# Kernel tuning notes

Hardware: AMD Instinct MI355X
Metric: run time of the kernel (lower is better)

Reference implementation:

```python
import jax, jax.numpy as jnp
import numpy as np
from jax import lax

B, IN_N, MID_N, OUT_N, K, L, WH = 16, 256, 256, 256, 3, 4096, 1024
EPS = 1e-5


def att_conv(x, W, b=None):
    # x: [B, Cin, L], W: [B, Cout, Cin, K] -> per-sample conv1d, padding='same'
    pl, pr = (K - 1) // 2, K // 2
    xp = jnp.pad(x, ((0, 0), (0, 0), (pl, pr)))
    out = 0.
    for t in range(K):  # small fixed K, unrolled shifted-slice einsum
        out = out + jnp.einsum('bcl,boc->bol', lax.dynamic_slice_in_dim(xp, t, L, 2), W[..., t])
    if b is not None:
        out = out + b[:, :, None]
    return out


def batch_norm(x, w, b):
    # training-mode BN over (N, L) per channel, biased variance
    mean = x.mean((0, 2), keepdims=True)
    var = ((x - mean) ** 2).mean((0, 2), keepdims=True)
    return (x - mean) * (w[None, :, None] / jnp.sqrt(var + EPS)) + b[None, :, None]


def se_module(x, w1, b1, w2, b2):
    s = x.mean(2, keepdims=True)  # [B, C, 1]
    s = jax.nn.relu(jnp.einsum('bcl,oc->bol', s, w1) + b1[None, :, None])
    s = jax.nn.sigmoid(jnp.einsum('bcl,oc->bol', s, w2) + b2[None, :, None])
    return x * s


def setup_inputs() -> dict:
    key = jax.random.key(0)
    ks = jax.random.split(key, 16)
    f = lambda k, sh, sc=0.02: jax.random.normal(k, sh, jnp.float32) * sc
    return {
        'x': f(ks[0], (B, IN_N, L), 1.0),
        'att1': f(ks[1], (B, MID_N, WH), 1.0),
        'att2': f(ks[2], (B, MID_N, WH), 1.0),
        'att3': f(ks[3], (B, OUT_N, WH), 1.0),
        'w1_w': f(ks[4], (IN_N * K, WH)), 'w1_b': jnp.zeros((IN_N * K,), jnp.float32),
        'w2_w': f(ks[5], (MID_N * K, WH)), 'w2_b': jnp.zeros((MID_N * K,), jnp.float32),
        'w3_w': f(ks[6], (MID_N * K, WH)), 'w3_b': jnp.zeros((MID_N * K,), jnp.float32),
        'b1_w': f(ks[7], (1, WH)), 'b1_b': jnp.zeros((1,), jnp.float32),
        'bn2_w': jnp.full((MID_N,), 0.1, jnp.float32), 'bn2_b': jnp.zeros((MID_N,), jnp.float32),
        'bn3_w': jnp.full((OUT_N,), 0.1, jnp.float32), 'bn3_b': jnp.zeros((OUT_N,), jnp.float32),
        'se1_w': f(ks[8], (OUT_N, OUT_N)), 'se1_b': jnp.zeros((OUT_N,), jnp.float32),
        'se2_w': f(ks[9], (OUT_N, OUT_N)), 'se2_b': jnp.zeros((OUT_N,), jnp.float32),
    }


def reference(x, att1, att2, att3, w1_w, w1_b, w2_w, w2_b, w3_w, w3_b,
              b1_w, b1_b, bn2_w, bn2_b, bn3_w, bn3_b, se1_w, se1_b, se2_w, se2_b):
    shortcut = x  # in_n == out_n, no downsample -> Identity
    # hypernetwork weight generation (Linear on last dim)
    W1 = (att1 @ w1_w.T + w1_b).reshape(B, MID_N, IN_N, K)
    W2 = (att2 @ w2_w.T + w2_b).reshape(B, MID_N, MID_N, K)
    W3 = (att3 @ w3_w.T + w3_b).reshape(B, OUT_N, MID_N, K)
    b1 = (att1 @ b1_w.T + b1_b)[..., 0]  # [B, mid_n]
    h = jax.nn.relu(att_conv(x, W1, b1))
    h = jax.nn.relu(batch_norm(att_conv(h, W2), bn2_w, bn2_b))
    h = jax.nn.relu(batch_norm(att_conv(h, W3), bn3_w, bn3_b))
    out = jax.nn.relu(se_module(h, se1_w, se1_b, se2_w, se2_b) + shortcut)
    return out
```

## Files before the change

### kernel.cpp

```cpp
#include <hip/hip_runtime.h>
#include <hip/hip_bf16.h>

using bf16 = __hip_bfloat16;
typedef __attribute__((ext_vector_type(4))) float f32x4;
typedef __attribute__((ext_vector_type(8))) short short8;
typedef __attribute__((ext_vector_type(2))) unsigned int uint2v;
typedef __attribute__((ext_vector_type(4))) unsigned int uint4v;

#define DEVI static __device__ __forceinline__

DEVI unsigned short f2b(float f){
  unsigned int u = __float_as_uint(f);
  unsigned int r = (u + 0x7fffu + ((u >> 16) & 1u)) >> 16;
  return (unsigned short)r;
}
DEVI float b2f(unsigned short u){
  return __uint_as_float(((unsigned int)u) << 16);
}

DEVI void gload16(const void* g, void* l){
  __builtin_amdgcn_global_load_lds(
      (const __attribute__((address_space(1))) unsigned int*)g,
      (__attribute__((address_space(3))) unsigned int*)l, 16, 0, 0);
}

__global__ __launch_bounds__(256) void k_transpose_x(const float* __restrict__ x,
                                                     bf16* __restrict__ xt)
{
  __shared__ float tile[64][65];
  const int b = blockIdx.z, l0 = blockIdx.x*64, c0 = blockIdx.y*64;
  const int tid = threadIdx.x;
  {
    const int r = tid >> 2, q = tid & 3;
    const float* src = x + ((size_t)(b*256 + c0 + r))*4096 + l0 + q*16;
    #pragma unroll
    for (int j = 0; j < 4; ++j){
      const f32x4 v = *reinterpret_cast<const f32x4*>(src + j*4);
      #pragma unroll
      for (int e = 0; e < 4; ++e) tile[r][q*16 + j*4 + e] = v[e];
    }
  }
  __syncthreads();
  {
    const int jr = tid >> 2, cq = tid & 3;
    unsigned int w[8];
    #pragma unroll
    for (int e = 0; e < 8; ++e){
      const float lo = tile[cq*16 + 2*e][jr];
      const float hi = tile[cq*16 + 2*e + 1][jr];
      w[e] = (unsigned int)f2b(lo) | ((unsigned int)f2b(hi) << 16);
    }
    unsigned short* dst = (unsigned short*)xt + ((size_t)b*4098 + l0 + jr + 1)*256 + c0 + cq*16;
    uint4v a0 = {w[0],w[1],w[2],w[3]}, a1 = {w[4],w[5],w[6],w[7]};
    *reinterpret_cast<uint4v*>(dst)     = a0;
    *reinterpret_cast<uint4v*>(dst + 8) = a1;
  }
}

__global__ void k_zero_pads(bf16* __restrict__ xt, bf16* __restrict__ h1t)
{
  const int b = blockIdx.x, tid = threadIdx.x;
  const size_t top = (size_t)b*4098*256 + tid;
  const size_t bot = (size_t)b*4098*256 + (size_t)4097*256 + tid;
  unsigned short* px = (unsigned short*)xt;
  unsigned short* ph = (unsigned short*)h1t;
  px[top] = 0; px[bot] = 0; ph[top] = 0; ph[bot] = 0;
}

__global__ __launch_bounds__(256) void k_cvt3(const float* __restrict__ s0, const float* __restrict__ s1,
                                              const float* __restrict__ s2, bf16* __restrict__ dst, int n1)
{
  const size_t total = (size_t)3 * (size_t)n1 / 4;
  for (size_t i = (size_t)blockIdx.x*256 + threadIdx.x; i < total; i += (size_t)gridDim.x*256){
    const size_t e = i*4;
    const int which = (int)(e / (size_t)n1);
    const size_t off = e - (size_t)which*(size_t)n1;
    const float* s = which==0 ? s0 : which==1 ? s1 : s2;
    const f32x4 v = *reinterpret_cast<const f32x4*>(s + off);
    uint2v p;
    p[0] = (unsigned)f2b(v[0]) | ((unsigned)f2b(v[1])<<16);
    p[1] = (unsigned)f2b(v[2]) | ((unsigned)f2b(v[3])<<16);
    *reinterpret_cast<uint2v*>((unsigned short*)dst + e) = p;
  }
}

__global__ __launch_bounds__(256, 3) void k_gen(const float* __restrict__ att1f, const float* __restrict__ att2f,
                                                const float* __restrict__ att3f, const bf16* __restrict__ wbp,
                                                const float* __restrict__ bias0, const float* __restrict__ bias1,
                                                const float* __restrict__ bias2, bf16* __restrict__ Wt)
{
  __shared__ bf16 sAll[24576];
  const int flat = blockIdx.x + blockIdx.z*64;
  const int xcd = flat & 7, s = flat >> 3;
  const int t = s % 3, u = s / 3;
  const int ch = u & 1;
  const int tau = (u >> 1)*8 + xcd;
  const int i = tau >> 5, boc = tau & 31;
  const int bo0 = boc*128, c0 = ch*128;
  const bf16*  __restrict__ A  = wbp + (size_t)i*768*1024 + (size_t)(c0*3 + t)*1024;
  const float* __restrict__ Bf = ((i==0) ? att1f : (i==1) ? att2f : att3f) + (size_t)bo0*1024;
  const float* __restrict__ bias = (i==0) ? bias0 : (i==1) ? bias1 : bias2;
  const int tid = threadIdx.x, lane = tid & 63, wid = tid >> 6;
  const int wr = wid >> 1, wc = wid & 1;
  const int frow = lane & 15, g = lane >> 4;
  f32x4 acc[4][4] = {};

#define GEN_STAGE(kt, bufi) { \
    _Pragma("unroll") \
    for (int j = 0; j < 2; ++j){ \
      const int q = tid + j*256, r = q >> 2, s3 = q & 3; \
      const int cc = (s3 ^ ((r >> 1) & 3)) * 8; \
      gload16(A + (size_t)r*3072 + (kt)*32 + cc, (char*)sAll + (bufi)*8192 + q*16); \
    } \
    _Pragma("unroll") \
    for (int j = 0; j < 4; ++j){ \
      const int q = tid + j*256, r = q >> 3, s7 = q & 7; \
      const int ss = s7 ^ (r & 7); \
      gload16(Bf + (size_t)r*1024 + (kt)*32 + ss*4, (char*)sAll + 16384 + (bufi)*16384 + q*16); \
    } \
  }

  GEN_STAGE(0, 0);
  #pragma unroll 1
  for (int kt = 0; kt < 32; ++kt){
    const int p = kt & 1;
    if (kt + 1 < 32){
      GEN_STAGE(kt+1, p^1);
      asm volatile("s_waitcnt vmcnt(6)" ::: "memory");
    } else {
      asm volatile("s_waitcnt vmcnt(0)" ::: "memory");
    }
    __builtin_amdgcn_s_barrier();
    const char* pA = (const char*)sAll + p*8192;
    const char* pB = (const char*)sAll + 16384 + p*16384;
    short8 bfr[4];
    #pragma unroll
    for (int n = 0; n < 4; ++n){
      const int row = wc*64 + n*16 + frow;
      const f32x4 f0 = *reinterpret_cast<const f32x4*>(pB + row*128 + (((2*g)  ^ (row & 7))*16));
      const f32x4 f1 = *reinterpret_cast<const f32x4*>(pB + row*128 + (((2*g+1)^ (row & 7))*16));
      unsigned int w0, w1, w2, w3;
      asm("v_cvt_pk_bf16_f32 %0, %1, %2" : "=v"(w0) : "v"(f0[0]), "v"(f0[1]));
      asm("v_cvt_pk_bf16_f32 %0, %1, %2" : "=v"(w1) : "v"(f0[2]), "v"(f0[3]));
      asm("v_cvt_pk_bf16_f32 %0, %1, %2" : "=v"(w2) : "v"(f1[0]), "v"(f1[1]));
      asm("v_cvt_pk_bf16_f32 %0, %1, %2" : "=v"(w3) : "v"(f1[2]), "v"(f1[3]));
      union { uint4v u; short8 sv; } cvtu;
      cvtu.u[0] = w0; cvtu.u[1] = w1; cvtu.u[2] = w2; cvtu.u[3] = w3;
      bfr[n] = cvtu.sv;
    }
    __builtin_amdgcn_s_setprio(1);
    #pragma unroll
    for (int m = 0; m < 4; ++m){
      const int row = wr*64 + m*16 + frow;
      const int sl = g ^ ((row >> 1) & 3);
      const short8 af = *reinterpret_cast<const short8*>(pA + row*64 + sl*16);
      #pragma unroll
      for (int n = 0; n < 4; ++n)
        acc[m][n] = __builtin_amdgcn_mfma_f32_16x16x32_bf16(af, bfr[n], acc[m][n], 0, 0, 0);
    }
    __builtin_amdgcn_s_setprio(0);
    __builtin_amdgcn_s_barrier();
  }
#undef GEN_STAGE

  #pragma unroll
  for (int m = 0; m < 4; ++m){
    const int lcol = wr*64 + m*16 + g*4;
    float bi[4];
    #pragma unroll
    for (int j = 0; j < 4; ++j) bi[j] = bias[(c0 + lcol + j)*3 + t];
    #pragma unroll
    for (int n = 0; n < 4; ++n){
      const int row = wc*64 + n*16 + frow;
      uint2v pk;
      pk[0] = (unsigned)f2b(acc[m][n][0] + bi[0]) | ((unsigned)f2b(acc[m][n][1] + bi[1]) << 16);
      pk[1] = (unsigned)f2b(acc[m][n][2] + bi[2]) | ((unsigned)f2b(acc[m][n][3] + bi[3]) << 16);
      const int chunk = (lcol >> 3) ^ (row & 15);
      *reinterpret_cast<uint2v*>((char*)sAll + row*256 + chunk*16 + (g&1)*8) = pk;
    }
  }
  __syncthreads();
  {
    const int bb = boc >> 1, o0 = (boc & 1)*128;
    char* gp = (char*)Wt + 2*(((((size_t)(i*16 + bb)*3 + t)*256 + o0)*256) + c0);
    #pragma unroll
    for (int it = 0; it < 8; ++it){
      const int row = it*16 + (tid >> 4);
      const int c = tid & 15;
      const int cs2 = c ^ (row & 15);
      const uint4v v = *reinterpret_cast<const uint4v*>((const char*)sAll + row*256 + cs2*16);
      *reinterpret_cast<uint4v*>(gp + (size_t)row*512 + c*16) = v;
    }
  }
}

__global__ __launch_bounds__(256) void k_b1(const float* __restrict__ att1, const float* __restrict__ b1w,
                                            const float* __restrict__ b1b, float* __restrict__ out)
{
  const int m = blockIdx.x*4 + (threadIdx.x >> 6);
  const int lane = threadIdx.x & 63;
  const float* a = att1 + (size_t)m*1024;
  float s = 0.f;
  for (int k = lane*4; k < 1024; k += 256){
    const f32x4 v = *reinterpret_cast<const f32x4*>(a + k);
    const f32x4 w = *reinterpret_cast<const f32x4*>(b1w + k);
    s += v[0]*w[0] + v[1]*w[1] + v[2]*w[2] + v[3]*w[3];
  }
  #pragma unroll
  for (int d = 32; d > 0; d >>= 1) s += __shfl_down(s, d);
  if (lane == 0) out[m] = s + b1b[0];
}

__global__ __launch_bounds__(512, 4) void k_conv(const bf16* __restrict__ Xt, const bf16* __restrict__ W,
                                                 const float* __restrict__ bias, bf16* __restrict__ out,
                                                 int outBatchStride, int outRowOff, int applyRelu,
                                                 float* __restrict__ statSum, float* __restrict__ statSq)
{
  __shared__ bf16 sAll[32768];
  const int flat = blockIdx.x + (blockIdx.z << 5);
  const int xcd = flat & 7, slot = flat >> 3;
  const int b = 2*xcd + (slot >> 5);
  const int l0 = (slot & 31) * 128;
  const int tid = threadIdx.x, lane = tid & 63, wid = tid >> 6;
  const int wr = wid >> 1, wc = wid & 1;
  const int frow = lane & 15, g = lane >> 4;
  f32x4 acc[4][4] = {};

#define CONV_STAGE(kt, bufi) { \
    const int ct3 = (kt)/3, tt = (kt) - ct3*3, c0 = ct3*32; \
    const bf16* Ab = W  + (((size_t)b*3 + tt)*256)*256 + c0; \
    const bf16* Bb = Xt + ((size_t)b*4098 + l0 + tt)*256 + c0; \
    _Pragma("unroll") \
    for (int j = 0; j < 2; ++j){ \
      const int q = tid + j*512, r = q >> 2, s3 = q & 3; \
      const int cc = (s3 ^ ((r >> 1) & 3)) * 8; \
      gload16(Ab + (size_t)r*256 + cc, &sAll[(bufi)*8192 + q*8]); \
    } \
    { const int q = tid, r = q >> 2, s3 = q & 3; \
      const int cc = (s3 ^ ((r >> 1) & 3)) * 8; \
      gload16(Bb + (size_t)r*256 + cc, &sAll[16384 + (bufi)*4096 + q*8]); } \
  }

  CONV_STAGE(0, 0);
  #pragma unroll 1
  for (int kt = 0; kt < 24; ++kt){
    const int buf = kt & 1;
    if (kt + 1 < 24){
      CONV_STAGE(kt+1, buf^1);
      asm volatile("s_waitcnt vmcnt(3)" ::: "memory");
    } else {
      asm volatile("s_waitcnt vmcnt(0)" ::: "memory");
    }
    __builtin_amdgcn_s_barrier();
    const bf16* pA = sAll + buf*8192;
    const bf16* pB = sAll + 16384 + buf*4096;
    short8 bfr[4], afr[4];
    #pragma unroll
    for (int n = 0; n < 4; ++n){
      const int row = wc*64 + n*16 + frow;
      const int sl = g ^ ((row >> 1) & 3);
      bfr[n] = *reinterpret_cast<const short8*>(pB + row*32 + sl*8);
    }
    #pragma unroll
    for (int m = 0; m < 4; ++m){
      const int row = wr*64 + m*16 + frow;
      const int sl = g ^ ((row >> 1) & 3);
      afr[m] = *reinterpret_cast<const short8*>(pA + row*32 + sl*8);
    }
    __builtin_amdgcn_s_setprio(1);
    #pragma unroll
    for (int m = 0; m < 4; ++m)
      #pragma unroll
      for (int n = 0; n < 4; ++n)
        acc[m][n] = __builtin_amdgcn_mfma_f32_16x16x32_bf16(afr[m], bfr[n], acc[m][n], 0, 0, 0);
    __builtin_amdgcn_s_setprio(0);
    __builtin_amdgcn_s_barrier();
  }
#undef CONV_STAGE

  float cs[4][4] = {{0.f}}, cq[4][4] = {{0.f}};
  #pragma unroll
  for (int m = 0; m < 4; ++m){
    const int col = wr*64 + m*16 + g*4;
    float bi[4] = {0.f, 0.f, 0.f, 0.f};
    if (bias){
      const f32x4 bv = *reinterpret_cast<const f32x4*>(bias + b*256 + col);
      bi[0]=bv[0]; bi[1]=bv[1]; bi[2]=bv[2]; bi[3]=bv[3];
    }
    #pragma unroll
    for (int n = 0; n < 4; ++n){
      const int row = wc*64 + n*16 + frow;
      float v[4];
      #pragma unroll
      for (int j = 0; j < 4; ++j){
        v[j] = acc[m][n][j] + bi[j];
        if (applyRelu) v[j] = fmaxf(v[j], 0.f);
        cs[m][j] += v[j];
        cq[m][j] += v[j]*v[j];
      }
      uint2v pk;
      pk[0] = (unsigned)f2b(v[0]) | ((unsigned)f2b(v[1]) << 16);
      pk[1] = (unsigned)f2b(v[2]) | ((unsigned)f2b(v[3]) << 16);
      const int chunk = (col >> 3) ^ (row & 31);
      *reinterpret_cast<uint2v*>((char*)sAll + row*512 + chunk*16 + (g&1)*8) = pk;
    }
  }
  __syncthreads();
  {
    char* gp = (char*)out + 2*((size_t)b*outBatchStride + (size_t)(l0 + outRowOff)*256);
    #pragma unroll
    for (int it = 0; it < 8; ++it){
      const int row = it*16 + (tid >> 5);
      const int c = tid & 31;
      const int cs2 = c ^ (row & 31);
      const uint4v v = *reinterpret_cast<const uint4v*>((const char*)sAll + row*512 + cs2*16);
      *reinterpret_cast<uint4v*>(gp + (size_t)row*512 + c*16) = v;
    }
  }
  if (statSum){
    #pragma unroll
    for (int m = 0; m < 4; ++m)
      #pragma unroll
      for (int j = 0; j < 4; ++j){
        #pragma unroll
        for (int d = 1; d < 16; d <<= 1){
          cs[m][j] += __shfl_xor(cs[m][j], d);
          cq[m][j] += __shfl_xor(cq[m][j], d);
        }
      }
    __syncthreads();
    float* ls = (float*)sAll;
    float* lq = ls + 512;
    if (frow == 0){
      #pragma unroll
      for (int m = 0; m < 4; ++m)
        #pragma unroll
        for (int j = 0; j < 4; ++j){
          ls[wid*64 + m*16 + g*4 + j] = cs[m][j];
          lq[wid*64 + m*16 + g*4 + j] = cq[m][j];
        }
    }
    __syncthreads();
    if (tid < 256){
      const int o = tid, wrI = o >> 6, idx = o & 63;
      const float s  = ls[(wrI*2 + 0)*64 + idx] + ls[(wrI*2 + 1)*64 + idx];
      const float qq = lq[(wrI*2 + 0)*64 + idx] + lq[(wrI*2 + 1)*64 + idx];
      atomicAdd(statSum + o, s);
      atomicAdd(statSq  + o, qq);
    }
  }
}

__global__ void k_bnfin(const float* __restrict__ sum, const float* __restrict__ sq,
                        const float* __restrict__ g, const float* __restrict__ bb,
                        float* __restrict__ scale, float* __restrict__ shift)
{
  const int o = threadIdx.x;
  const float inv = 1.f/65536.f;
  const float m = sum[o]*inv;
  const float v = fmaxf(sq[o]*inv - m*m, 0.f);
  const float sc = g[o] / sqrtf(v + 1e-5f);
  scale[o] = sc;
  shift[o] = bb[o] - m*sc;
}

__global__ __launch_bounds__(256) void k_norm2(const bf16* __restrict__ y, const float* __restrict__ scale,
                                               const float* __restrict__ shift, bf16* __restrict__ h)
{
  const int gr = blockIdx.x*8 + (threadIdx.x >> 5);
  const int oc = threadIdx.x & 31;
  const int b = gr / 4098, lp = gr - b*4098;
  unsigned short* dst = (unsigned short*)h + (size_t)gr*256 + oc*8;
  if (lp == 0 || lp == 4097){
    uint4v z = {0u,0u,0u,0u};
    *reinterpret_cast<uint4v*>(dst) = z;
    return;
  }
  const unsigned short* src = (const unsigned short*)y + ((size_t)b*4096 + (lp-1))*256 + oc*8;
  const uint4v in = *reinterpret_cast<const uint4v*>(src);
  const f32x4 sA0 = *reinterpret_cast<const f32x4*>(scale + oc*8);
  const f32x4 sA1 = *reinterpret_cast<const f32x4*>(scale + oc*8 + 4);
  const f32x4 hA0 = *reinterpret_cast<const f32x4*>(shift + oc*8);
  const f32x4 hA1 = *reinterpret_cast<const f32x4*>(shift + oc*8 + 4);
  uint4v ov;
  #pragma unroll
  for (int e = 0; e < 4; ++e){
    const unsigned int w = in[e];
    const float sc0 = (e<2) ? sA0[2*e] : sA1[2*e-4];
    const float sc1 = (e<2) ? sA0[2*e+1] : sA1[2*e-3];
    const float sh0 = (e<2) ? hA0[2*e] : hA1[2*e-4];
    const float sh1 = (e<2) ? hA0[2*e+1] : hA1[2*e-3];
    const float v0 = fmaxf(b2f((unsigned short)(w & 0xffffu))*sc0 + sh0, 0.f);
    const float v1 = fmaxf(b2f((unsigned short)(w >> 16))*sc1 + sh1, 0.f);
    ov[e] = (unsigned)f2b(v0) | ((unsigned)f2b(v1) << 16);
  }
  *reinterpret_cast<uint4v*>(dst) = ov;
}

__global__ __launch_bounds__(256) void k_norm3(bf16* __restrict__ y, const float* __restrict__ scale,
                                               const float* __restrict__ shift, float* __restrict__ s_sum)
{
  __shared__ float red[8][256];
  const int tid = threadIdx.x;
  const int rr = tid >> 5, oc = tid & 31;
  const size_t row = (size_t)blockIdx.x*8 + rr;
  const int b = (int)(row >> 12);
  unsigned short* p = (unsigned short*)y + row*256 + oc*8;
  const uint4v in = *reinterpret_cast<const uint4v*>(p);
  const f32x4 sA0 = *reinterpret_cast<const f32x4*>(scale + oc*8);
  const f32x4 sA1 = *reinterpret_cast<const f32x4*>(scale + oc*8 + 4);
  const f32x4 hA0 = *reinterpret_cast<const f32x4*>(shift + oc*8);
  const f32x4 hA1 = *reinterpret_cast<const f32x4*>(shift + oc*8 + 4);
  uint4v ov;
  float loc[8];
  #pragma unroll
  for (int e = 0; e < 4; ++e){
    const unsigned int w = in[e];
    const float sc0 = (e<2) ? sA0[2*e] : sA1[2*e-4];
    const float sc1 = (e<2) ? sA0[2*e+1] : sA1[2*e-3];
    const float sh0 = (e<2) ? hA0[2*e] : hA1[2*e-4];
    const float sh1 = (e<2) ? hA0[2*e+1] : hA1[2*e-3];
    const float v0 = fmaxf(b2f((unsigned short)(w & 0xffffu))*sc0 + sh0, 0.f);
    const float v1 = fmaxf(b2f((unsigned short)(w >> 16))*sc1 + sh1, 0.f);
    loc[2*e] = v0; loc[2*e+1] = v1;
    ov[e] = (unsigned)f2b(v0) | ((unsigned)f2b(v1) << 16);
  }
  *reinterpret_cast<uint4v*>(p) = ov;
  #pragma unroll
  for (int j = 0; j < 8; ++j) red[rr][oc*8 + j] = loc[j];
  __syncthreads();
  const int o = tid;
  float tot = 0.f;
  #pragma unroll
  for (int r2 = 0; r2 < 8; ++r2) tot += red[r2][o];
  atomicAdd(&s_sum[(size_t)b*256 + o], tot);
}

__global__ __launch_bounds__(256) void k_se(const float* __restrict__ s_sum, const float* __restrict__ w1,
                                            const float* __restrict__ b1, const float* __restrict__ w2,
                                            const float* __restrict__ b2, float* __restrict__ s2)
{
  __shared__ float sv[256];
  __shared__ float t1[256];
  const int b = blockIdx.x, o = threadIdx.x;
  sv[o] = s_sum[(size_t)b*256 + o] * (1.f/4096.f);
  __syncthreads();
  float a = b1[o];
  for (int c = 0; c < 256; ++c) a += w1[(size_t)o*256 + c] * sv[c];
  t1[o] = fmaxf(a, 0.f);
  __syncthreads();
  float a2 = b2[o];
  for (int c = 0; c < 256; ++c) a2 += w2[(size_t)o*256 + c] * t1[c];
  s2[(size_t)b*256 + o] = 1.f / (1.f + expf(-a2));
}

__global__ __launch_bounds__(256) void k_final(const bf16* __restrict__ h3, const float* __restrict__ s2,
                                               const float* __restrict__ x, float* __restrict__ out)
{
  __shared__ float tile[64][65];
  const int b = blockIdx.z, o0 = blockIdx.y*64, l0 = blockIdx.x*64;
  const int tid = threadIdx.x;
  {
    const int r = tid >> 2, q = tid & 3;
    const unsigned short* src = (const unsigned short*)h3 + ((size_t)b*4096 + l0 + r)*256 + o0 + q*16;
    const uint4v a0 = *reinterpret_cast<const uint4v*>(src);
    const uint4v a1 = *reinterpret_cast<const uint4v*>(src + 8);
    #pragma unroll
    for (int e = 0; e < 4; ++e){
      tile[r][q*16 + 2*e]         = b2f((unsigned short)(a0[e] & 0xffffu));
      tile[r][q*16 + 2*e + 1]     = b2f((unsigned short)(a0[e] >> 16));
      tile[r][q*16 + 8 + 2*e]     = b2f((unsigned short)(a1[e] & 0xffffu));
      tile[r][q*16 + 8 + 2*e + 1] = b2f((unsigned short)(a1[e] >> 16));
    }
  }
  __syncthreads();
  {
    const int orow = tid >> 2, q = tid & 3;
    const int o = o0 + orow;
    const float sc = s2[(size_t)b*256 + o];
    const float* xs = x + ((size_t)b*256 + o)*4096 + l0 + q*16;
    float* dst = out + ((size_t)b*256 + o)*4096 + l0 + q*16;
    #pragma unroll
    for (int k = 0; k < 16; k += 4){
      const f32x4 xv = *reinterpret_cast<const f32x4*>(xs + k);
      f32x4 r;
      #pragma unroll
      for (int e = 0; e < 4; ++e)
        r[e] = fmaxf(tile[q*16 + k + e][orow]*sc + xv[e], 0.f);
      *reinterpret_cast<f32x4*>(dst + k) = r;
    }
  }
}

extern "C" void kernel_launch(void* const* d_in, const int* in_sizes, int n_in,
                              void* d_out, int out_size, void* d_ws, size_t ws_size,
                              hipStream_t stream)
{
  const float* x     = (const float*)d_in[0];
  const float* att1  = (const float*)d_in[1];
  const float* att2  = (const float*)d_in[2];
  const float* att3  = (const float*)d_in[3];
  const float* w1_w  = (const float*)d_in[4];
  const float* w1_b  = (const float*)d_in[5];
  const float* w2_w  = (const float*)d_in[6];
  const float* w2_b  = (const float*)d_in[7];
  const float* w3_w  = (const float*)d_in[8];
  const float* w3_b  = (const float*)d_in[9];
  const float* b1_w  = (const float*)d_in[10];
  const float* b1_b  = (const float*)d_in[11];
  const float* bn2_w = (const float*)d_in[12];
  const float* bn2_b = (const float*)d_in[13];
  const float* bn3_w = (const float*)d_in[14];
  const float* bn3_b = (const float*)d_in[15];
  const float* se1_w = (const float*)d_in[16];
  const float* se1_b = (const float*)d_in[17];
  const float* se2_w = (const float*)d_in[18];
  const float* se2_b = (const float*)d_in[19];

  char* ws = (char*)d_ws;
  bf16*  xT   = (bf16*)(ws + 0);
  bf16*  h1T  = (bf16*)(ws + 33570816);
  bf16*  y2T  = (bf16*)(ws + 67141632);
  bf16*  h2T  = (bf16*)(ws + 100696064);
  bf16*  Wt   = (bf16*)(ws + 134266880);
  bf16*  wb   = (bf16*)(ws + 178307072);
  float* b1v  = (float*)(ws + 183025664);
  float* st   = (float*)(ws + 183042048);
  float* bn2sum = st;
  float* bn2sq  = st + 256;
  float* bn3sum = st + 512;
  float* bn3sq  = st + 768;
  float* s_sum  = st + 1024;
  float* scale2 = st + 5120;
  float* shift2 = st + 5376;
  float* scale3 = st + 5632;
  float* shift3 = st + 5888;
  float* s2v    = st + 6144;
  bf16*  y3T  = (bf16*)(ws + 0);

  hipMemsetAsync(st, 0, 5120*sizeof(float), stream);

  k_transpose_x<<<dim3(64,4,16),256,0,stream>>>(x, xT);
  k_zero_pads<<<16,256,0,stream>>>(xT, h1T);
  k_cvt3<<<512,256,0,stream>>>(w1_w, w2_w, w3_w, wb, 768*1024);
  k_gen<<<dim3(64,1,9),256,0,stream>>>(att1, att2, att3, wb, w1_b, w2_b, w3_b, Wt);
  k_b1<<<1024,256,0,stream>>>(att1, b1_w, b1_b, b1v);

  k_conv<<<dim3(32,1,16),512,0,stream>>>(xT,  Wt,                           b1v,     h1T, 4098*256, 1, 1, nullptr, nullptr);
  k_conv<<<dim3(32,1,16),512,0,stream>>>(h1T, Wt + (size_t)1*16*3*256*256,  nullptr, y2T, 4096*256, 0, 0, bn2sum, bn2sq);
  k_bnfin<<<1,256,0,stream>>>(bn2sum, bn2sq, bn2_w, bn2_b, scale2, shift2);
  k_norm2<<<8196,256,0,stream>>>(y2T, scale2, shift2, h2T);
  k_conv<<<dim3(32,1,16),512,0,stream>>>(h2T, Wt + (size_t)2*16*3*256*256,  nullptr, y3T, 4096*256, 0, 0, bn3sum, bn3sq);
  k_bnfin<<<1,256,0,stream>>>(bn3sum, bn3sq, bn3_w, bn3_b, scale3, shift3);
  k_norm3<<<8192,256,0,stream>>>(y3T, scale3, shift3, s_sum);
  k_se<<<16,256,0,stream>>>(s_sum, se1_w, se1_b, se2_w, se2_b, s2v);
  k_final<<<dim3(64,4,16),256,0,stream>>>((const bf16*)y3T, s2v, x, (float*)d_out);
}
```

Baseline: 309.2 us.

## Enlarge conv tile to 256x256 with 64-wide K steps and interleaved staging

Result: no change. 307.6 us (-0.5%).

```diff
diff --git a/kernel.cpp b/kernel.cpp
--- a/kernel.cpp
+++ b/kernel.cpp
@@ -211,77 +211,106 @@
   if (lane == 0) out[m] = s + b1b[0];
 }
 
-__global__ __launch_bounds__(512, 4) void k_conv(const bf16* __restrict__ Xt, const bf16* __restrict__ W,
+__global__ __launch_bounds__(512, 2) void k_conv(const bf16* __restrict__ Xt, const bf16* __restrict__ W,
                                                  const float* __restrict__ bias, bf16* __restrict__ out,
                                                  int outBatchStride, int outRowOff, int applyRelu,
                                                  float* __restrict__ statSum, float* __restrict__ statSq)
 {
-  __shared__ bf16 sAll[32768];
-  const int flat = blockIdx.x + (blockIdx.z << 5);
-  const int xcd = flat & 7, slot = flat >> 3;
-  const int b = 2*xcd + (slot >> 5);
-  const int l0 = (slot & 31) * 128;
+  __shared__ bf16 sAll[65536];
+  const int flat = blockIdx.x + (blockIdx.z << 4);
+  const int xcd = flat & 7, sl_ = flat >> 3;
+  const int b = 2*xcd + (sl_ >> 4);
+  const int l0 = (sl_ & 15) * 256;
   const int tid = threadIdx.x, lane = tid & 63, wid = tid >> 6;
-  const int wr = wid >> 1, wc = wid & 1;
+  const int wr = wid >> 2, wc = wid & 3;
   const int frow = lane & 15, g = lane >> 4;
-  f32x4 acc[4][4] = {};
-
-#define CONV_STAGE(kt, bufi) { \
-    const int ct3 = (kt)/3, tt = (kt) - ct3*3, c0 = ct3*32; \
-    const bf16* Ab = W  + (((size_t)b*3 + tt)*256)*256 + c0; \
-    const bf16* Bb = Xt + ((size_t)b*4098 + l0 + tt)*256 + c0; \
+  f32x4 acc[8][4] = {};
+
+  const int r0 = tid >> 3,        cc0 = ((tid & 7) ^ (r0 & 7));
+  const int r1 = (tid+512) >> 3,  cc1 = (((tid+512) & 7) ^ (r1 & 7));
+
+#define BARR asm volatile("s_barrier" ::: "memory")
+
+#define STG_A(j, h) { const int t_=(j)%3, c0_=((j)/3)*64; \
+    const bf16* gp_ = W + (((size_t)b*3 + t_)*256 + (h)*128)*256 + c0_; \
+    char* lb_ = (char*)sAll + (((j)&1)*32768) + (h)*16384; \
+    gload16(gp_ + (size_t)r0*256 + cc0*8, lb_ + tid*16); \
+    gload16(gp_ + (size_t)r1*256 + cc1*8, lb_ + (tid+512)*16); }
+
+#define STG_B(j, h) { const int t_=(j)%3, c0_=((j)/3)*64; \
+    const bf16* gp_ = Xt + ((size_t)b*4098 + l0 + t_ + (h)*128)*256 + c0_; \
+    char* lb_ = (char*)sAll + 65536 + (((j)&1)*32768) + (h)*16384; \
+    gload16(gp_ + (size_t)r0*256 + cc0*8, lb_ + tid*16); \
+    gload16(gp_ + (size_t)r1*256 + cc1*8, lb_ + (tid+512)*16); }
+
+#define RD_A(j, mh) { const char* pa_ = (const char*)sAll + (((j)&1)*32768) + wr*16384; \
     _Pragma("unroll") \
-    for (int j = 0; j < 2; ++j){ \
-      const int q = tid + j*512, r = q >> 2, s3 = q & 3; \
-      const int cc = (s3 ^ ((r >> 1) & 3)) * 8; \
-      gload16(Ab + (size_t)r*256 + cc, &sAll[(bufi)*8192 + q*8]); \
-    } \
-    { const int q = tid, r = q >> 2, s3 = q & 3; \
-      const int cc = (s3 ^ ((r >> 1) & 3)) * 8; \
-      gload16(Bb + (size_t)r*256 + cc, &sAll[16384 + (bufi)*4096 + q*8]); } \
-  }
-
-  CONV_STAGE(0, 0);
+    for (int mf = 0; mf < 4; ++mf){ const int rowl = ((mh)*4 + mf)*16 + frow; \
+      _Pragma("unroll") \
+      for (int ks = 0; ks < 2; ++ks) \
+        afr[mf][ks] = *reinterpret_cast<const short8*>(pa_ + rowl*128 + (((ks*4+g) ^ (rowl & 7))*16)); } }
+
+#define RD_B(j) { const char* pb_ = (const char*)sAll + 65536 + (((j)&1)*32768) + (wc>>1)*16384; \
+    _Pragma("unroll") \
+    for (int nf = 0; nf < 4; ++nf){ const int rowl = (wc&1)*64 + nf*16 + frow; \
+      _Pragma("unroll") \
+      for (int ks = 0; ks < 2; ++ks) \
+        bfr[nf][ks] = *reinterpret_cast<const short8*>(pb_ + rowl*128 + (((ks*4+g) ^ (rowl & 7))*16)); } }
+
+#define MFMA16(mh, ks) { __builtin_amdgcn_s_setprio(1); \
+    _Pragma("unroll") \
+    for (int mf = 0; mf < 4; ++mf) \
+      _Pragma("unroll") \
+      for (int nf = 0; nf < 4; ++nf) \
+        acc[(mh)*4+mf][nf] = __builtin_amdgcn_mfma_f32_16x16x32_bf16(afr[mf][ks], bfr[nf][ks], acc[(mh)*4+mf][nf], 0, 0, 0); \
+    __builtin_amdgcn_s_setprio(0); }
+
+  STG_A(0,0); STG_A(0,1); STG_B(0,0); STG_B(0,1);
+  STG_A(1,0); STG_A(1,1); STG_B(1,0); STG_B(1,1);
+  asm volatile("s_waitcnt vmcnt(0)" ::: "memory");
+  BARR;
+
+  short8 afr[4][2], bfr[4][2];
   #pragma unroll 1
-  for (int kt = 0; kt < 24; ++kt){
-    const int buf = kt & 1;
-    if (kt + 1 < 24){
-      CONV_STAGE(kt+1, buf^1);
-      asm volatile("s_waitcnt vmcnt(3)" ::: "memory");
-    } else {
-      asm volatile("s_waitcnt vmcnt(0)" ::: "memory");
-    }
-    __builtin_amdgcn_s_barrier();
-    const bf16* pA = sAll + buf*8192;
-    const bf16* pB = sAll + 16384 + buf*4096;
-    short8 bfr[4], afr[4];
-    #pragma unroll
-    for (int n = 0; n < 4; ++n){
-      const int row = wc*64 + n*16 + frow;
-      const int sl = g ^ ((row >> 1) & 3);
-      bfr[n] = *reinterpret_cast<const short8*>(pB + row*32 + sl*8);
-    }
-    #pragma unroll
-    for (int m = 0; m < 4; ++m){
-      const int row = wr*64 + m*16 + frow;
-      const int sl = g ^ ((row >> 1) & 3);
-      afr[m] = *reinterpret_cast<const short8*>(pA + row*32 + sl*8);
-    }
-    __builtin_amdgcn_s_setprio(1);
-    #pragma unroll
-    for (int m = 0; m < 4; ++m)
-      #pragma unroll
-      for (int n = 0; n < 4; ++n)
-        acc[m][n] = __builtin_amdgcn_mfma_f32_16x16x32_bf16(afr[m], bfr[n], acc[m][n], 0, 0, 0);
-    __builtin_amdgcn_s_setprio(0);
-    __builtin_amdgcn_s_barrier();
-  }
-#undef CONV_STAGE
-
-  float cs[4][4] = {{0.f}}, cq[4][4] = {{0.f}};
-  #pragma unroll
-  for (int m = 0; m < 4; ++m){
-    const int col = wr*64 + m*16 + g*4;
+  for (int i = 0; i < 6; ++i){
+    const int J0 = 2*i, J1 = 2*i + 1;
+    const bool st = (i < 5);
+    RD_A(J0, 0); RD_B(J0);
+    if (i > 0) STG_A(J1, 1);
+    BARR; MFMA16(0, 0); BARR;
+    if (st) STG_B(J0+2, 0);
+    BARR; MFMA16(0, 1); BARR;
+    RD_A(J0, 1);
+    if (st) STG_B(J0+2, 1);
+    BARR; MFMA16(1, 0); BARR;
+    if (st) STG_A(J0+2, 0);
+    if (st) { asm volatile("s_waitcnt vmcnt(6)" ::: "memory"); }
+    else    { asm volatile("s_waitcnt vmcnt(0)" ::: "memory"); }
+    BARR; MFMA16(1, 1); BARR;
+    RD_A(J1, 0); RD_B(J1);
+    if (st) STG_A(J0+2, 1);
+    BARR; MFMA16(0, 0); BARR;
+    if (st) STG_B(J1+2, 0);
+    BARR; MFMA16(0, 1); BARR;
+    RD_A(J1, 1);
+    if (st) STG_B(J1+2, 1);
+    BARR; MFMA16(1, 0); BARR;
+    if (st) STG_A(J1+2, 0);
+    if (st) { asm volatile("s_waitcnt vmcnt(6)" ::: "memory"); }
+    else    { asm volatile("s_waitcnt vmcnt(0)" ::: "memory"); }
+    BARR; MFMA16(1, 1); BARR;
+  }
+#undef STG_A
+#undef STG_B
+#undef RD_A
+#undef RD_B
+#undef MFMA16
+#undef BARR
+
+  float cs[8][4] = {{0.f}}, cq[8][4] = {{0.f}};
+  #pragma unroll
+  for (int m = 0; m < 8; ++m){
+    const int col = wr*128 + m*16 + g*4;
     float bi[4] = {0.f, 0.f, 0.f, 0.f};
     if (bias){
       const f32x4 bv = *reinterpret_cast<const f32x4*>(bias + b*256 + col);
@@ -298,19 +327,19 @@
         cs[m][j] += v[j];
         cq[m][j] += v[j]*v[j];
       }
-      uint2v pk;
-      pk[0] = (unsigned)f2b(v[0]) | ((unsigned)f2b(v[1]) << 16);
-      pk[1] = (unsigned)f2b(v[2]) | ((unsigned)f2b(v[3]) << 16);
+      uint2v p;
+      p[0] = (unsigned)f2b(v[0]) | ((unsigned)f2b(v[1]) << 16);
+      p[1] = (unsigned)f2b(v[2]) | ((unsigned)f2b(v[3]) << 16);
       const int chunk = (col >> 3) ^ (row & 31);
-      *reinterpret_cast<uint2v*>((char*)sAll + row*512 + chunk*16 + (g&1)*8) = pk;
+      *reinterpret_cast<uint2v*>((char*)sAll + row*512 + chunk*16 + (g&1)*8) = p;
     }
   }
   __syncthreads();
   {
     char* gp = (char*)out + 2*((size_t)b*outBatchStride + (size_t)(l0 + outRowOff)*256);
     #pragma unroll
-    for (int it = 0; it < 8; ++it){
-      const int row = it*16 + (tid >> 5);
+    for (int p2 = 0; p2 < 16; ++p2){
+      const int row = p2*16 + (tid >> 5);
       const int c = tid & 31;
       const int cs2 = c ^ (row & 31);
       const uint4v v = *reinterpret_cast<const uint4v*>((const char*)sAll + row*512 + cs2*16);
@@ -319,7 +348,7 @@
   }
   if (statSum){
     #pragma unroll
-    for (int m = 0; m < 4; ++m)
+    for (int m = 0; m < 8; ++m)
       #pragma unroll
       for (int j = 0; j < 4; ++j){
         #pragma unroll
@@ -330,21 +359,25 @@
       }
     __syncthreads();
     float* ls = (float*)sAll;
-    float* lq = ls + 512;
+    float* lq = ls + 1024;
     if (frow == 0){
       #pragma unroll
-      for (int m = 0; m < 4; ++m)
+      for (int m = 0; m < 8; ++m)
         #pragma unroll
         for (int j = 0; j < 4; ++j){
-          ls[wid*64 + m*16 + g*4 + j] = cs[m][j];
-          lq[wid*64 + m*16 + g*4 + j] = cq[m][j];
+          ls[wid*128 + m*16 + g*4 + j] = cs[m][j];
+          lq[wid*128 + m*16 + g*4 + j] = cq[m][j];
         }
     }
     __syncthreads();
     if (tid < 256){
-      const int o = tid, wrI = o >> 6, idx = o & 63;
-      const float s  = ls[(wrI*2 + 0)*64 + idx] + ls[(wrI*2 + 1)*64 + idx];
-      const float qq = lq[(wrI*2 + 0)*64 + idx] + lq[(wrI*2 + 1)*64 + idx];
+      const int o = tid, half = o >> 7, idx = o & 127;
+      float s = 0.f, qq = 0.f;
+      #pragma unroll
+      for (int wv = 0; wv < 4; ++wv){
+        s  += ls[(half*4 + wv)*128 + idx];
+        qq += lq[(half*4 + wv)*128 + idx];
+      }
       atomicAdd(statSum + o, s);
       atomicAdd(statSq  + o, qq);
     }
@@ -546,11 +579,11 @@
   k_gen<<<dim3(64,1,9),256,0,stream>>>(att1, att2, att3, wb, w1_b, w2_b, w3_b, Wt);
   k_b1<<<1024,256,0,stream>>>(att1, b1_w, b1_b, b1v);
 
-  k_conv<<<dim3(32,1,16),512,0,stream>>>(xT,  Wt,                           b1v,     h1T, 4098*256, 1, 1, nullptr, nullptr);
-  k_conv<<<dim3(32,1,16),512,0,stream>>>(h1T, Wt + (size_t)1*16*3*256*256,  nullptr, y2T, 4096*256, 0, 0, bn2sum, bn2sq);
+  k_conv<<<dim3(16,1,16),512,0,stream>>>(xT,  Wt,                           b1v,     h1T, 4098*256, 1, 1, nullptr, nullptr);
+  k_conv<<<dim3(16,1,16),512,0,stream>>>(h1T, Wt + (size_t)1*16*3*256*256,  nullptr, y2T, 4096*256, 0, 0, bn2sum, bn2sq);
   k_bnfin<<<1,256,0,stream>>>(bn2sum, bn2sq, bn2_w, bn2_b, scale2, shift2);
   k_norm2<<<8196,256,0,stream>>>(y2T, scale2, shift2, h2T);
-  k_conv<<<dim3(32,1,16),512,0,stream>>>(h2T, Wt + (size_t)2*16*3*256*256,  nullptr, y3T, 4096*256, 0, 0, bn3sum, bn3sq);
+  k_conv<<<dim3(16,1,16),512,0,stream>>>(h2T, Wt + (size_t)2*16*3*256*256,  nullptr, y3T, 4096*256, 0, 0, bn3sum, bn3sq);
   k_bnfin<<<1,256,0,stream>>>(bn3sum, bn3sq, bn3_w, bn3_b, scale3, shift3);
   k_norm3<<<8192,256,0,stream>>>(y3T, scale3, shift3, s_sum);
   k_se<<<16,256,0,stream>>>(s_sum, se1_w, se1_b, se2_w, se2_b, s2v);
```
